# Kernel tuning notes

Hardware: AMD Instinct MI355X
Metric: run time of the kernel (lower is better)

Reference implementation:

```python
import jax, jax.numpy as jnp
import numpy as np

B, D, S, SE, H, DFF = 4, 1024, 1024, 1024, 16, 4096
DH = D // H
NUDGE = 1e-7


def norm(x):
    # x: [B, D, S]; custom layer norm: mean over (1,2), then divide by full L2 norm
    size = x.shape[1] * x.shape[2]
    mean = jnp.sum(x, axis=(1, 2)) / size
    x = x - mean[:, None, None]
    std = jnp.sqrt(jnp.sum(x * x, axis=(1, 2)))
    return x / (std[:, None, None] + NUDGE)


def mha(q_in, kv_in, Wq, Wk, Wv, Wo, causal):
    # q_in: [B, Sq, D], kv_in: [B, Sk, D]
    Bq, Sq, _ = q_in.shape
    Sk = kv_in.shape[1]
    q = (q_in @ Wq).reshape(Bq, Sq, H, DH)
    k = (kv_in @ Wk).reshape(Bq, Sk, H, DH)
    v = (kv_in @ Wv).reshape(Bq, Sk, H, DH)
    scores = jnp.einsum('bqhd,bkhd->bhqk', q, k) / jnp.sqrt(jnp.asarray(DH, q.dtype))
    if causal:
        mask = jnp.tril(jnp.ones((Sq, Sk), dtype=bool))
        scores = jnp.where(mask, scores, jnp.finfo(scores.dtype).min)
    attn = jax.nn.softmax(scores, axis=-1)
    out = jnp.einsum('bhqk,bkhd->bqhd', attn, v).reshape(Bq, Sq, D)
    return out @ Wo


def setup_inputs() -> dict:
    key = jax.random.key(0)
    ks = jax.random.split(key, 13)
    w = lambda k, sh: jax.random.normal(k, sh, dtype=jnp.float32) * 0.02
    return {
        'embedding': jax.random.normal(ks[0], (B, D, SE), dtype=jnp.float32),
        'other_inputs': jax.random.normal(ks[1], (B, D, S), dtype=jnp.float32),
        'Wq_s': w(ks[2], (D, D)), 'Wk_s': w(ks[3], (D, D)),
        'Wv_s': w(ks[4], (D, D)), 'Wo_s': w(ks[5], (D, D)),
        'Wq_c': w(ks[6], (D, D)), 'Wk_c': w(ks[7], (D, D)),
        'Wv_c': w(ks[8], (D, D)), 'Wo_c': w(ks[9], (D, D)),
        'W1': w(ks[10], (D, DFF)), 'b1': jnp.zeros((DFF,), jnp.float32),
        'W2': w(ks[11], (DFF, D)), 'b2': jnp.zeros((D,), jnp.float32),
    }


def reference(embedding, other_inputs, Wq_s, Wk_s, Wv_s, Wo_s,
              Wq_c, Wk_c, Wv_c, Wo_c, W1, b1, W2, b2):
    # tensors are [B, D, S]; attention operates on [B, S, D]
    x = other_inputs.transpose(0, 2, 1)
    sa = mha(x, x, Wq_s, Wk_s, Wv_s, Wo_s, causal=True)
    post_attention = norm(other_inputs + sa.transpose(0, 2, 1))

    pa = post_attention.transpose(0, 2, 1)
    emb = embedding.transpose(0, 2, 1)
    ca = mha(pa, emb, Wq_c, Wk_c, Wv_c, Wo_c, causal=False)
    post_embedding = norm(post_attention + ca.transpose(0, 2, 1))

    # per-token MLP (original loops over axis 2 and restacks; here fully batched)
    pe = post_embedding.transpose(0, 2, 1)  # [B, S, D]
    ff = jax.nn.relu(pe @ W1 + b1) @ W2 + b2
    return norm(post_embedding + ff.transpose(0, 2, 1))
```

## Files before the change

### kernel.cpp

```cpp
#include <hip/hip_runtime.h>
#include <cmath>

#define B_   4
#define D_   1024
#define S_   1024
#define H_   16
#define DH_  64
#define DFF_ 4096

typedef __attribute__((ext_vector_type(8))) short bf16x8;
typedef __attribute__((ext_vector_type(4))) float f32x4;

__device__ __forceinline__ unsigned short f2b(float f) {
    unsigned int u = __float_as_uint(f);
    u += 0x7fffu + ((u >> 16) & 1u);
    return (unsigned short)(u >> 16);
}

__device__ __forceinline__ void gload_lds16(const unsigned short* g, unsigned short* l) {
    __builtin_amdgcn_global_load_lds(
        (const __attribute__((address_space(1))) void*)g,
        (__attribute__((address_space(3))) void*)l, 16, 0, 0);
}

template <int BM, int BN, bool RES>
__global__ __launch_bounds__(256, 2)
void gemm_t(const unsigned short* __restrict__ A,
            const unsigned short* __restrict__ Wt,
            const float* __restrict__ bias,
            const float* __restrict__ residual,
            float* __restrict__ Cf, unsigned short* __restrict__ Cb,
            float* __restrict__ partial,
            int N, int K, int lda, int ldb, long csplit, int relu)
{
    constexpr int FM = BM / 32, FN = BN / 32;
    __shared__ unsigned short As[BM * 64];
    __shared__ unsigned short Bs[BN * 64];
    const int tid = threadIdx.x;
    const int w = tid >> 6, lane = tid & 63;
    const int quad = lane >> 4, l16 = lane & 15;
    const int m0 = blockIdx.x * BM, n0 = blockIdx.y * BN;
    const int wm = (w >> 1) * (BM / 2), wn = (w & 1) * (BN / 2);
    const int srow = lane >> 3;
    const int scol = ((lane & 7) ^ srow) * 8;

    A  += (size_t)blockIdx.z * K;
    Wt += (size_t)blockIdx.z * K;
    if (Cf) Cf += (size_t)blockIdx.z * csplit;

    f32x4 acc[FM][FN] = {};

    for (int k0 = 0; k0 < K; k0 += 64) {
#pragma unroll
        for (int i = 0; i < BM / 32; ++i) {
            const int inst = w + 4 * i;
            gload_lds16(A + (size_t)(m0 + inst * 8 + srow) * lda + k0 + scol,
                        As + inst * 512);
        }
#pragma unroll
        for (int i = 0; i < BN / 32; ++i) {
            const int inst = w + 4 * i;
            gload_lds16(Wt + (size_t)(n0 + inst * 8 + srow) * ldb + k0 + scol,
                        Bs + inst * 512);
        }
        __syncthreads();

#pragma unroll
        for (int kk = 0; kk < 2; ++kk) {
            bf16x8 af[FM], bfr[FN];
#pragma unroll
            for (int i = 0; i < FM; ++i) {
                const int r = wm + i * 16 + l16;
                af[i] = *(const bf16x8*)&As[r * 64 + (((kk * 4 + quad) ^ (r & 7)) * 8)];
            }
#pragma unroll
            for (int j = 0; j < FN; ++j) {
                const int r = wn + j * 16 + l16;
                bfr[j] = *(const bf16x8*)&Bs[r * 64 + (((kk * 4 + quad) ^ (r & 7)) * 8)];
            }
#pragma unroll
            for (int i = 0; i < FM; ++i)
#pragma unroll
                for (int j = 0; j < FN; ++j)
                    acc[i][j] = __builtin_amdgcn_mfma_f32_16x16x32_bf16(af[i], bfr[j], acc[i][j], 0, 0, 0);
        }
        __syncthreads();
    }

    float s = 0.f, ss = 0.f;
#pragma unroll
    for (int i = 0; i < FM; ++i) {
        const int grow = m0 + wm + i * 16 + quad * 4;
#pragma unroll
        for (int j = 0; j < FN; ++j) {
            const int gcol = n0 + wn + j * 16 + l16;
            const float bv = bias ? bias[gcol] : 0.f;
#pragma unroll
            for (int r = 0; r < 4; ++r) {
                float vv = acc[i][j][r] + bv;
                if (relu) vv = fmaxf(vv, 0.f);
                if constexpr (RES) {
                    vv += residual[(size_t)(grow + r) * N + gcol];
                    s += vv; ss += vv * vv;
                    Cf[(size_t)(grow + r) * N + gcol] = vv;
                } else {
                    if (Cf) Cf[(size_t)(grow + r) * N + gcol] = vv;
                    if (Cb) Cb[(size_t)(grow + r) * N + gcol] = f2b(vv);
                }
            }
        }
    }

    if constexpr (RES) {
        float* rs = (float*)As;
        float* rss = rs + 256;
        rs[tid] = s; rss[tid] = ss;
        __syncthreads();
        for (int off = 128; off > 0; off >>= 1) {
            if (tid < off) { rs[tid] += rs[tid + off]; rss[tid] += rss[tid + off]; }
            __syncthreads();
        }
        if (tid == 0) {
            constexpr int YPB = S_ / BM;
            const int b = blockIdx.x / YPB;
            const int chunk = (blockIdx.x % YPB) * gridDim.y + blockIdx.y;
            const int chunks = YPB * gridDim.y;
            partial[((size_t)b * chunks + chunk) * 2 + 0] = rs[0];
            partial[((size_t)b * chunks + chunk) * 2 + 1] = rss[0];
        }
    }
}

__global__ void reduce2_res(const float* __restrict__ pc, const float* __restrict__ res,
                            const float* __restrict__ bias, float* __restrict__ y,
                            float* __restrict__ partial)
{
    const size_t pcs = (size_t)4096 * 1024;
    const int b = blockIdx.y;
    const size_t base = (size_t)b * 1048576 + (size_t)blockIdx.x * 16384;
    float s = 0.f, ss = 0.f;
    for (int i = threadIdx.x; i < 4096; i += 256) {
        const size_t e = base + (size_t)i * 4;
        float4 v0 = *(const float4*)&pc[e];
        float4 v1 = *(const float4*)&pc[e + pcs];
        float4 rv = *(const float4*)&res[e];
        float4 bv = *(const float4*)&bias[e & 1023];
        float4 o;
        o.x = v0.x + v1.x + rv.x + bv.x;
        o.y = v0.y + v1.y + rv.y + bv.y;
        o.z = v0.z + v1.z + rv.z + bv.z;
        o.w = v0.w + v1.w + rv.w + bv.w;
        *(float4*)&y[e] = o;
        s += o.x + o.y + o.z + o.w;
        ss += o.x * o.x + o.y * o.y + o.z * o.z + o.w * o.w;
    }
    __shared__ float rs[256], rss[256];
    rs[threadIdx.x] = s; rss[threadIdx.x] = ss;
    __syncthreads();
    for (int off = 128; off > 0; off >>= 1) {
        if (threadIdx.x < off) {
            rs[threadIdx.x] += rs[threadIdx.x + off];
            rss[threadIdx.x] += rss[threadIdx.x + off];
        }
        __syncthreads();
    }
    if (threadIdx.x == 0) {
        partial[((size_t)b * 64 + blockIdx.x) * 2 + 0] = rs[0];
        partial[((size_t)b * 64 + blockIdx.x) * 2 + 1] = rss[0];
    }
}

__device__ __forceinline__ void stats_reduce(const float* __restrict__ partial,
                                             int b, int chunks, int tid,
                                             float* rs, float* rss,
                                             float& mean, float& inv)
{
    float s = 0.f, ss = 0.f;
    for (int i = tid; i < chunks; i += 256) {
        s  += partial[((size_t)b * chunks + i) * 2 + 0];
        ss += partial[((size_t)b * chunks + i) * 2 + 1];
    }
    rs[tid] = s; rss[tid] = ss;
    __syncthreads();
    for (int off = 128; off > 0; off >>= 1) {
        if (tid < off) { rs[tid] += rs[tid + off]; rss[tid] += rss[tid + off]; }
        __syncthreads();
    }
    const float size = (float)(D_ * S_);
    const float m = rs[0] / size;
    const float var = fmaxf(rss[0] - size * m * m, 0.f);
    mean = m;
    inv = 1.f / (sqrtf(var) + 1e-7f);
    __syncthreads();
}

__global__ void norm_apply_dual(float* __restrict__ y, unsigned short* __restrict__ yb,
                                const float* __restrict__ partial, int chunks)
{
    __shared__ float rs[256], rss[256];
    const int b = blockIdx.y;
    float mean, inv;
    stats_reduce(partial, b, chunks, threadIdx.x, rs, rss, mean, inv);

    const int perBatch = D_ * S_;
    float4* y4 = (float4*)(y + (size_t)b * perBatch);
    unsigned short* yb_ = yb + (size_t)b * perBatch;
    const int n4 = perBatch / 4;
    for (int i = blockIdx.x * blockDim.x + threadIdx.x; i < n4;
         i += gridDim.x * blockDim.x) {
        float4 v = y4[i];
        v.x = (v.x - mean) * inv; v.y = (v.y - mean) * inv;
        v.z = (v.z - mean) * inv; v.w = (v.w - mean) * inv;
        y4[i] = v;
        ushort4 hh; hh.x = f2b(v.x); hh.y = f2b(v.y); hh.z = f2b(v.z); hh.w = f2b(v.w);
        *(ushort4*)(yb_ + (size_t)i * 4) = hh;
    }
}

template <bool CAUSAL>
__global__ __launch_bounds__(256, 2)
void attn_mfma3(const unsigned short* __restrict__ q, const unsigned short* __restrict__ k,
                const unsigned short* __restrict__ vt, unsigned short* __restrict__ o,
                int qstride, int kstride)
{
    __shared__ unsigned short Ks[128 * 64];
    __shared__ unsigned short Vt[64 * 128];
    __shared__ unsigned short Ps[4][2][16][72];
    const int tid = threadIdx.x;
    const int w = tid >> 6, lane = tid & 63;
    const int quad = lane >> 4, l16 = lane & 15;
    const int h = blockIdx.y, b = blockIdx.z;
    const int qt = CAUSAL ? ((blockIdx.x + h) & 7) : blockIdx.x;
    const int q0 = qt * 128;

    const int ksr = lane >> 3, ksc = ((lane & 7) ^ (lane >> 3)) * 8;
    const int vsr = lane >> 4, vsc = lane & 15;

    const unsigned short* qA = q + (size_t)(b * S_ + q0 + w * 16 + l16) * qstride + h * DH_;
    const unsigned short* qB = qA + (size_t)64 * qstride;
    const bf16x8 qa0 = *(const bf16x8*)(qA + quad * 8);
    const bf16x8 qa1 = *(const bf16x8*)(qA + 32 + quad * 8);
    const bf16x8 qb0 = *(const bf16x8*)(qB + quad * 8);
    const bf16x8 qb1 = *(const bf16x8*)(qB + 32 + quad * 8);

    f32x4 OA[4] = {}, OB[4] = {};
    float lA[4] = {}, lB[4] = {};

    const int nit = CAUSAL ? (qt + 1) : (S_ / 128);
    for (int t = 0; t < nit; ++t) {
        const int j0 = t * 128;
#pragma unroll
        for (int i = 0; i < 4; ++i) {
            const int ins = w + 4 * i;
            gload_lds16(k + (size_t)(b * S_ + j0 + ins * 8 + ksr) * kstride + h * DH_ + ksc,
                        Ks + ins * 512);
            const int vrow = ins * 4 + vsr;
            gload_lds16(vt + (size_t)((b * H_ + h) * DH_ + vrow) * S_ + j0
                           + ((vsc ^ (vrow & 15)) * 8),
                        Vt + ins * 512);
        }
        __syncthreads();

#pragma unroll
        for (int g = 0; g < 2; ++g) {
            const int kb = 2 * t + g;
            const int jg = j0 + g * 64;
            const bool doA = !CAUSAL || (kb <= 2 * qt);
            const bool diagA = CAUSAL && (kb == 2 * qt);
            const bool diagB = CAUSAL && (kb == 2 * qt + 1);

            f32x4 stA[4], stB[4];
#pragma unroll
            for (int n = 0; n < 4; ++n) {
                const int kr = g * 64 + n * 16 + l16;
                const bf16x8 kf0 = *(const bf16x8*)&Ks[kr * 64 + ((quad ^ (kr & 7)) * 8)];
                const bf16x8 kf1 = *(const bf16x8*)&Ks[kr * 64 + (((quad + 4) ^ (kr & 7)) * 8)];
                if (doA) {
                    f32x4 c = {};
                    c = __builtin_amdgcn_mfma_f32_16x16x32_bf16(qa0, kf0, c, 0, 0, 0);
                    c = __builtin_amdgcn_mfma_f32_16x16x32_bf16(qa1, kf1, c, 0, 0, 0);
                    stA[n] = c;
                }
                f32x4 c = {};
                c = __builtin_amdgcn_mfma_f32_16x16x32_bf16(qb0, kf0, c, 0, 0, 0);
                c = __builtin_amdgcn_mfma_f32_16x16x32_bf16(qb1, kf1, c, 0, 0, 0);
                stB[n] = c;
            }

            if (doA) {
#pragma unroll
                for (int n = 0; n < 4; ++n)
#pragma unroll
                    for (int r = 0; r < 4; ++r) {
                        float sv = stA[n][r] * 0.125f;
                        if (diagA) {
                            const int row = q0 + w * 16 + quad * 4 + r;
                            const int key = jg + n * 16 + l16;
                            if (key > row) sv = -1e30f;
                        }
                        const float p = __expf(sv);
                        lA[r] += p;
                        Ps[w][0][quad * 4 + r][n * 16 + l16] = f2b(p);
                    }
            }
#pragma unroll
            for (int n = 0; n < 4; ++n)
#pragma unroll
                for (int r = 0; r < 4; ++r) {
                    float sv = stB[n][r] * 0.125f;
                    if (diagB) {
                        const int row = q0 + 64 + w * 16 + quad * 4 + r;
                        const int key = jg + n * 16 + l16;
                        if (key > row) sv = -1e30f;
                    }
                    const float p = __expf(sv);
                    lB[r] += p;
                    Ps[w][1][quad * 4 + r][n * 16 + l16] = f2b(p);
                }
            __threadfence_block();

            const bf16x8 pa0 = *(const bf16x8*)&Ps[w][0][l16][quad * 8];
            const bf16x8 pa1 = *(const bf16x8*)&Ps[w][0][l16][32 + quad * 8];
            const bf16x8 pb0 = *(const bf16x8*)&Ps[w][1][l16][quad * 8];
            const bf16x8 pb1 = *(const bf16x8*)&Ps[w][1][l16][32 + quad * 8];
#pragma unroll
            for (int n = 0; n < 4; ++n) {
                const int vr = n * 16 + l16;
                const bf16x8 vf0 = *(const bf16x8*)&Vt[vr * 128 + (((g * 8 + quad) ^ l16) * 8)];
                const bf16x8 vf1 = *(const bf16x8*)&Vt[vr * 128 + (((g * 8 + quad + 4) ^ l16) * 8)];
                if (doA) {
                    OA[n] = __builtin_amdgcn_mfma_f32_16x16x32_bf16(pa0, vf0, OA[n], 0, 0, 0);
                    OA[n] = __builtin_amdgcn_mfma_f32_16x16x32_bf16(pa1, vf1, OA[n], 0, 0, 0);
                }
                OB[n] = __builtin_amdgcn_mfma_f32_16x16x32_bf16(pb0, vf0, OB[n], 0, 0, 0);
                OB[n] = __builtin_amdgcn_mfma_f32_16x16x32_bf16(pb1, vf1, OB[n], 0, 0, 0);
            }
        }
        __syncthreads();
    }

#pragma unroll
    for (int r = 0; r < 4; ++r) {
        float la = lA[r], lb = lB[r];
        la += __shfl_xor(la, 1); la += __shfl_xor(la, 2);
        la += __shfl_xor(la, 4); la += __shfl_xor(la, 8);
        lb += __shfl_xor(lb, 1); lb += __shfl_xor(lb, 2);
        lb += __shfl_xor(lb, 4); lb += __shfl_xor(lb, 8);
        const float ia = 1.f / la, ib = 1.f / lb;
        const size_t baseA = (size_t)(b * S_ + q0 + w * 16 + quad * 4 + r) * D_ + h * DH_;
        const size_t baseB = baseA + (size_t)64 * D_;
#pragma unroll
        for (int n = 0; n < 4; ++n) {
            o[baseA + n * 16 + l16] = f2b(OA[n][r] * ia);
            o[baseB + n * 16 + l16] = f2b(OB[n][r] * ib);
        }
    }
}

__global__ void transpose_v(const unsigned short* __restrict__ src,
                            unsigned short* __restrict__ dst, int istride)
{
    __shared__ unsigned short t[32][34];
    const int z = blockIdx.z, b = z >> 4, h = z & 15;
    const int s0 = blockIdx.x * 32, d0 = blockIdx.y * 32;
    const int tx = threadIdx.x, ty = threadIdx.y;
#pragma unroll
    for (int i = 0; i < 4; ++i)
        t[ty + i * 8][tx] =
            src[(size_t)(b * S_ + s0 + ty + i * 8) * istride + h * DH_ + d0 + tx];
    __syncthreads();
#pragma unroll
    for (int i = 0; i < 4; ++i)
        dst[(size_t)(z * DH_ + d0 + ty + i * 8) * S_ + s0 + tx] = t[tx][ty + i * 8];
}

struct WJob { const float* src; int sld; long doff; int dld; };
struct WJobs { WJob j[16]; };

__global__ void wtrans_all(WJobs js, unsigned short* __restrict__ dst)
{
    __shared__ float tile[32][33];
    const WJob J = js.j[blockIdx.z];
    const int c0 = blockIdx.x * 32, r0 = blockIdx.y * 32;
    const int tx = threadIdx.x, ty = threadIdx.y;
#pragma unroll
    for (int i = 0; i < 4; ++i)
        tile[ty + i * 8][tx] = J.src[(size_t)(r0 + ty + i * 8) * J.sld + c0 + tx];
    __syncthreads();
#pragma unroll
    for (int i = 0; i < 4; ++i)
        dst[J.doff + (size_t)(c0 + ty + i * 8) * J.dld + r0 + tx] =
            f2b(tile[tx][ty + i * 8]);
}

__global__ void transpose_in(const float* __restrict__ other, const float* __restrict__ emb,
                             float* __restrict__ f0, unsigned short* __restrict__ xb,
                             unsigned short* __restrict__ eb)
{
    __shared__ float tile[32][33];
    const int z = blockIdx.z;
    const int b = z & 3;
    const bool isEmb = z >= 4;
    const float* ip = (isEmb ? emb : other) + (size_t)b * 1048576;
    const int c0 = blockIdx.x * 32, r0 = blockIdx.y * 32;
    const int tx = threadIdx.x, ty = threadIdx.y;
#pragma unroll
    for (int i = 0; i < 4; ++i)
        tile[ty + i * 8][tx] = ip[(size_t)(r0 + ty + i * 8) * 1024 + c0 + tx];
    __syncthreads();
#pragma unroll
    for (int i = 0; i < 4; ++i) {
        const float v = tile[tx][ty + i * 8];
        const size_t oidx = (size_t)b * 1048576 + (size_t)(c0 + ty + i * 8) * 1024 + r0 + tx;
        if (isEmb) eb[oidx] = f2b(v);
        else { f0[oidx] = v; xb[oidx] = f2b(v); }
    }
}

__global__ void transpose_out(const float* __restrict__ in, float* __restrict__ outf,
                              const float* __restrict__ partial, int chunks)
{
    __shared__ float tile[32][33];
    __shared__ float rs[256], rss[256];
    const int z = blockIdx.z;
    const int tx = threadIdx.x, ty = threadIdx.y;
    const int tid = ty * 32 + tx;

    float mean, inv;
    stats_reduce(partial, z, chunks, tid, rs, rss, mean, inv);

    const float* ip = in + (size_t)z * 1048576;
    const int c0 = blockIdx.x * 32, r0 = blockIdx.y * 32;
#pragma unroll
    for (int i = 0; i < 4; ++i)
        tile[ty + i * 8][tx] = ip[(size_t)(r0 + ty + i * 8) * 1024 + c0 + tx];
    __syncthreads();
#pragma unroll
    for (int i = 0; i < 4; ++i) {
        const float v = (tile[tx][ty + i * 8] - mean) * inv;
        outf[(size_t)z * 1048576 + (size_t)(c0 + ty + i * 8) * 1024 + r0 + tx] = v;
    }
}

extern "C" void kernel_launch(void* const* d_in, const int* in_sizes, int n_in,
                              void* d_out, int out_size, void* d_ws, size_t ws_size,
                              hipStream_t stream)
{
    const float* embedding = (const float*)d_in[0];
    const float* other     = (const float*)d_in[1];
    const float* W1 = (const float*)d_in[10];
    const float* b1 = (const float*)d_in[11];
    const float* W2 = (const float*)d_in[12];
    const float* b2 = (const float*)d_in[13];
    float* out = (float*)d_out;

    char* wsb = (char*)d_ws;
    const size_t MB = 1u << 20;
    float* f0 = (float*)(wsb + 0 * MB);
    float* f2 = (float*)(wsb + 16 * MB);
    unsigned short* wts  = (unsigned short*)(wsb + 32 * MB);
    unsigned short* wqkv = wts;
    unsigned short* wo_s = wts + 3 * 1048576;
    unsigned short* wq_c = wts + 4 * 1048576;
    unsigned short* wkv_c= wts + 5 * 1048576;
    unsigned short* wo_c = wts + 7 * 1048576;
    unsigned short* w1t  = wts + 8 * 1048576;
    unsigned short* w2t  = wts + 12 * 1048576;
    unsigned short* actA = (unsigned short*)(wsb + 64 * MB);
    unsigned short* actB = (unsigned short*)(wsb + 72 * MB);
    unsigned short* actC = (unsigned short*)(wsb + 80 * MB);
    unsigned short* actC2 = actC + 4 * 1048576;
    unsigned short* aout  = actC + 12 * 1048576;
    float* pc      = (float*)(wsb + 112 * MB);
    float* partial = (float*)(wsb + 176 * MB);

    const dim3 blkT(32, 8), blk256(256);
    const dim3 gAttn(S_ / 128, H_, B_);
    const dim3 gVt(32, 2, B_ * H_);
    const dim3 gApply(64, B_);

    WJobs js;
    for (int z = 0; z < 8; ++z)
        js.j[z] = { (const float*)d_in[2 + z], 1024, (long)z * 1048576, 1024 };
    for (int q = 0; q < 4; ++q)
        js.j[8 + q] = { W1 + (size_t)q * 1024, 4096, (long)(8 + q) * 1048576, 1024 };
    for (int q = 0; q < 4; ++q)
        js.j[12 + q] = { W2 + (size_t)q * 1048576, 1024, 12L * 1048576 + q * 1024, 4096 };
    hipLaunchKernelGGL(wtrans_all, dim3(32, 32, 16), blkT, 0, stream, js, wts);

    hipLaunchKernelGGL(transpose_in, dim3(32, 32, 8), blkT, 0, stream,
                       other, embedding, f0, actA, actB);

    hipLaunchKernelGGL((gemm_t<128, 128, false>), dim3(32, 24), blk256, 0, stream,
                       actA, wqkv, nullptr, nullptr, nullptr, actC, nullptr,
                       3072, 1024, 1024, 1024, 0L, 0);
    hipLaunchKernelGGL(transpose_v, gVt, blkT, 0, stream, actC + 2048, actA, 3072);
    hipLaunchKernelGGL(attn_mfma3<true>, gAttn, blk256, 0, stream,
                       actC, actC + 1024, actA, aout, 3072, 3072);
    hipLaunchKernelGGL((gemm_t<64, 128, true>), dim3(64, 8), blk256, 0, stream,
                       aout, wo_s, nullptr, f0, f2, nullptr, partial,
                       1024, 1024, 1024, 1024, 0L, 0);
    hipLaunchKernelGGL(norm_apply_dual, gApply, blk256, 0, stream, f2, actA, partial, 128);

    hipLaunchKernelGGL((gemm_t<64, 128, false>), dim3(64, 8), blk256, 0, stream,
                       actA, wq_c, nullptr, nullptr, nullptr, actC, nullptr,
                       1024, 1024, 1024, 1024, 0L, 0);
    hipLaunchKernelGGL((gemm_t<128, 128, false>), dim3(32, 16), blk256, 0, stream,
                       actB, wkv_c, nullptr, nullptr, nullptr, actC2, nullptr,
                       2048, 1024, 1024, 1024, 0L, 0);
    hipLaunchKernelGGL(transpose_v, gVt, blkT, 0, stream, actC2 + 1024, actB, 2048);
    hipLaunchKernelGGL(attn_mfma3<false>, gAttn, blk256, 0, stream,
                       actC, actC2, actB, aout, 1024, 2048);
    hipLaunchKernelGGL((gemm_t<64, 128, true>), dim3(64, 8), blk256, 0, stream,
                       aout, wo_c, nullptr, f2, f0, nullptr, partial,
                       1024, 1024, 1024, 1024, 0L, 0);
    hipLaunchKernelGGL(norm_apply_dual, gApply, blk256, 0, stream, f0, actA, partial, 128);

    hipLaunchKernelGGL((gemm_t<128, 128, false>), dim3(32, 32), blk256, 0, stream,
                       actA, w1t, b1, nullptr, nullptr, actC, nullptr,
                       DFF_, 1024, 1024, 1024, 0L, 1);
    hipLaunchKernelGGL((gemm_t<128, 128, false>), dim3(32, 8, 2), blk256, 0, stream,
                       actC, w2t, nullptr, nullptr, pc, nullptr, nullptr,
                       1024, 2048, 4096, 4096, (long)4096 * 1024, 0);
    hipLaunchKernelGGL(reduce2_res, gApply, blk256, 0, stream, pc, f0, b2, f2, partial);
    hipLaunchKernelGGL(transpose_out, dim3(32, 32, B_), blkT, 0, stream, f2, out, partial, 64);

    (void)in_sizes; (void)n_in; (void)out_size; (void)ws_size;
}
```

Before: 503.5 us.

## Split attention query tile across 8 waves instead of 4 with two sub-tiles each

```diff
diff --git a/kernel.cpp b/kernel.cpp
--- a/kernel.cpp
+++ b/kernel.cpp
@@ -218,40 +218,38 @@
 }
 
 template <bool CAUSAL>
-__global__ __launch_bounds__(256, 2)
+__global__ __launch_bounds__(512, 4)
 void attn_mfma3(const unsigned short* __restrict__ q, const unsigned short* __restrict__ k,
                 const unsigned short* __restrict__ vt, unsigned short* __restrict__ o,
                 int qstride, int kstride)
 {
     __shared__ unsigned short Ks[128 * 64];
     __shared__ unsigned short Vt[64 * 128];
-    __shared__ unsigned short Ps[4][2][16][72];
+    __shared__ unsigned short Ps[8][16][72];
     const int tid = threadIdx.x;
     const int w = tid >> 6, lane = tid & 63;
     const int quad = lane >> 4, l16 = lane & 15;
     const int h = blockIdx.y, b = blockIdx.z;
     const int qt = CAUSAL ? ((blockIdx.x + h) & 7) : blockIdx.x;
     const int q0 = qt * 128;
+    const int row0 = q0 + w * 16;
 
     const int ksr = lane >> 3, ksc = ((lane & 7) ^ (lane >> 3)) * 8;
     const int vsr = lane >> 4, vsc = lane & 15;
 
-    const unsigned short* qA = q + (size_t)(b * S_ + q0 + w * 16 + l16) * qstride + h * DH_;
-    const unsigned short* qB = qA + (size_t)64 * qstride;
+    const unsigned short* qA = q + (size_t)(b * S_ + row0 + l16) * qstride + h * DH_;
     const bf16x8 qa0 = *(const bf16x8*)(qA + quad * 8);
     const bf16x8 qa1 = *(const bf16x8*)(qA + 32 + quad * 8);
-    const bf16x8 qb0 = *(const bf16x8*)(qB + quad * 8);
-    const bf16x8 qb1 = *(const bf16x8*)(qB + 32 + quad * 8);
-
-    f32x4 OA[4] = {}, OB[4] = {};
-    float lA[4] = {}, lB[4] = {};
+
+    f32x4 OA[4] = {};
+    float lA[4] = {};
 
     const int nit = CAUSAL ? (qt + 1) : (S_ / 128);
     for (int t = 0; t < nit; ++t) {
         const int j0 = t * 128;
 #pragma unroll
-        for (int i = 0; i < 4; ++i) {
-            const int ins = w + 4 * i;
+        for (int i = 0; i < 2; ++i) {
+            const int ins = w + 8 * i;
             gload_lds16(k + (size_t)(b * S_ + j0 + ins * 8 + ksr) * kstride + h * DH_ + ksc,
                         Ks + ins * 512);
             const int vrow = ins * 4 + vsr;
@@ -263,77 +261,49 @@
 
 #pragma unroll
         for (int g = 0; g < 2; ++g) {
-            const int kb = 2 * t + g;
             const int jg = j0 + g * 64;
-            const bool doA = !CAUSAL || (kb <= 2 * qt);
-            const bool diagA = CAUSAL && (kb == 2 * qt);
-            const bool diagB = CAUSAL && (kb == 2 * qt + 1);
-
-            f32x4 stA[4], stB[4];
-#pragma unroll
-            for (int n = 0; n < 4; ++n) {
-                const int kr = g * 64 + n * 16 + l16;
-                const bf16x8 kf0 = *(const bf16x8*)&Ks[kr * 64 + ((quad ^ (kr & 7)) * 8)];
-                const bf16x8 kf1 = *(const bf16x8*)&Ks[kr * 64 + (((quad + 4) ^ (kr & 7)) * 8)];
-                if (doA) {
+            const bool doW = !CAUSAL || (jg <= row0 + 15);
+            const bool needMask = CAUSAL && doW && (jg + 63 > row0);
+
+            if (doW) {
+                f32x4 stA[4];
+#pragma unroll
+                for (int n = 0; n < 4; ++n) {
+                    const int kr = g * 64 + n * 16 + l16;
+                    const bf16x8 kf0 = *(const bf16x8*)&Ks[kr * 64 + ((quad ^ (kr & 7)) * 8)];
+                    const bf16x8 kf1 = *(const bf16x8*)&Ks[kr * 64 + (((quad + 4) ^ (kr & 7)) * 8)];
                     f32x4 c = {};
                     c = __builtin_amdgcn_mfma_f32_16x16x32_bf16(qa0, kf0, c, 0, 0, 0);
                     c = __builtin_amdgcn_mfma_f32_16x16x32_bf16(qa1, kf1, c, 0, 0, 0);
                     stA[n] = c;
                 }
-                f32x4 c = {};
-                c = __builtin_amdgcn_mfma_f32_16x16x32_bf16(qb0, kf0, c, 0, 0, 0);
-                c = __builtin_amdgcn_mfma_f32_16x16x32_bf16(qb1, kf1, c, 0, 0, 0);
-                stB[n] = c;
-            }
-
-            if (doA) {
+
 #pragma unroll
                 for (int n = 0; n < 4; ++n)
 #pragma unroll
                     for (int r = 0; r < 4; ++r) {
                         float sv = stA[n][r] * 0.125f;
-                        if (diagA) {
-                            const int row = q0 + w * 16 + quad * 4 + r;
+                        if (needMask) {
+                            const int row = row0 + quad * 4 + r;
                             const int key = jg + n * 16 + l16;
                             if (key > row) sv = -1e30f;
                         }
                         const float p = __expf(sv);
                         lA[r] += p;
-                        Ps[w][0][quad * 4 + r][n * 16 + l16] = f2b(p);
+                        Ps[w][quad * 4 + r][n * 16 + l16] = f2b(p);
                     }
-            }
-#pragma unroll
-            for (int n = 0; n < 4; ++n)
-#pragma unroll
-                for (int r = 0; r < 4; ++r) {
-                    float sv = stB[n][r] * 0.125f;
-                    if (diagB) {
-                        const int row = q0 + 64 + w * 16 + quad * 4 + r;
-                        const int key = jg + n * 16 + l16;
-                        if (key > row) sv = -1e30f;
-                    }
-                    const float p = __expf(sv);
-                    lB[r] += p;
-                    Ps[w][1][quad * 4 + r][n * 16 + l16] = f2b(p);
-                }
-            __threadfence_block();
-
-            const bf16x8 pa0 = *(const bf16x8*)&Ps[w][0][l16][quad * 8];
-            const bf16x8 pa1 = *(const bf16x8*)&Ps[w][0][l16][32 + quad * 8];
-            const bf16x8 pb0 = *(const bf16x8*)&Ps[w][1][l16][quad * 8];
-            const bf16x8 pb1 = *(const bf16x8*)&Ps[w][1][l16][32 + quad * 8];
-#pragma unroll
-            for (int n = 0; n < 4; ++n) {
-                const int vr = n * 16 + l16;
-                const bf16x8 vf0 = *(const bf16x8*)&Vt[vr * 128 + (((g * 8 + quad) ^ l16) * 8)];
-                const bf16x8 vf1 = *(const bf16x8*)&Vt[vr * 128 + (((g * 8 + quad + 4) ^ l16) * 8)];
-                if (doA) {
+                __threadfence_block();
+
+                const bf16x8 pa0 = *(const bf16x8*)&Ps[w][l16][quad * 8];
+                const bf16x8 pa1 = *(const bf16x8*)&Ps[w][l16][32 + quad * 8];
+#pragma unroll
+                for (int n = 0; n < 4; ++n) {
+                    const int vr = n * 16 + l16;
+                    const bf16x8 vf0 = *(const bf16x8*)&Vt[vr * 128 + (((g * 8 + quad) ^ l16) * 8)];
+                    const bf16x8 vf1 = *(const bf16x8*)&Vt[vr * 128 + (((g * 8 + quad + 4) ^ l16) * 8)];
                     OA[n] = __builtin_amdgcn_mfma_f32_16x16x32_bf16(pa0, vf0, OA[n], 0, 0, 0);
                     OA[n] = __builtin_amdgcn_mfma_f32_16x16x32_bf16(pa1, vf1, OA[n], 0, 0, 0);
                 }
-                OB[n] = __builtin_amdgcn_mfma_f32_16x16x32_bf16(pb0, vf0, OB[n], 0, 0, 0);
-                OB[n] = __builtin_amdgcn_mfma_f32_16x16x32_bf16(pb1, vf1, OB[n], 0, 0, 0);
             }
         }
         __syncthreads();
@@ -341,19 +311,14 @@
 
 #pragma unroll
     for (int r = 0; r < 4; ++r) {
-        float la = lA[r], lb = lB[r];
+        float la = lA[r];
         la += __shfl_xor(la, 1); la += __shfl_xor(la, 2);
         la += __shfl_xor(la, 4); la += __shfl_xor(la, 8);
-        lb += __shfl_xor(lb, 1); lb += __shfl_xor(lb, 2);
-        lb += __shfl_xor(lb, 4); lb += __shfl_xor(lb, 8);
-        const float ia = 1.f / la, ib = 1.f / lb;
-        const size_t baseA = (size_t)(b * S_ + q0 + w * 16 + quad * 4 + r) * D_ + h * DH_;
-        const size_t baseB = baseA + (size_t)64 * D_;
-#pragma unroll
-        for (int n = 0; n < 4; ++n) {
+        const float ia = 1.f / la;
+        const size_t baseA = (size_t)(b * S_ + row0 + quad * 4 + r) * D_ + h * DH_;
+#pragma unroll
+        for (int n = 0; n < 4; ++n)
             o[baseA + n * 16 + l16] = f2b(OA[n][r] * ia);
-            o[baseB + n * 16 + l16] = f2b(OB[n][r] * ib);
-        }
     }
 }
 
@@ -474,7 +439,7 @@
     float* pc      = (float*)(wsb + 112 * MB);
     float* partial = (float*)(wsb + 176 * MB);
 
-    const dim3 blkT(32, 8), blk256(256);
+    const dim3 blkT(32, 8), blk256(256), blk512(512);
     const dim3 gAttn(S_ / 128, H_, B_);
     const dim3 gVt(32, 2, B_ * H_);
     const dim3 gApply(64, B_);
@@ -495,7 +460,7 @@
                        actA, wqkv, nullptr, nullptr, nullptr, actC, nullptr,
                        3072, 1024, 1024, 1024, 0L, 0);
     hipLaunchKernelGGL(transpose_v, gVt, blkT, 0, stream, actC + 2048, actA, 3072);
-    hipLaunchKernelGGL(attn_mfma3<true>, gAttn, blk256, 0, stream,
+    hipLaunchKernelGGL(attn_mfma3<true>, gAttn, blk512, 0, stream,
                        actC, actC + 1024, actA, aout, 3072, 3072);
     hipLaunchKernelGGL((gemm_t<64, 128, true>), dim3(64, 8), blk256, 0, stream,
                        aout, wo_s, nullptr, f0, f2, nullptr, partial,
@@ -509,7 +474,7 @@
                        actB, wkv_c, nullptr, nullptr, nullptr, actC2, nullptr,
                        2048, 1024, 1024, 1024, 0L, 0);
     hipLaunchKernelGGL(transpose_v, gVt, blkT, 0, stream, actC2 + 1024, actB, 2048);
-    hipLaunchKernelGGL(attn_mfma3<false>, gAttn, blk256, 0, stream,
+    hipLaunchKernelGGL(attn_mfma3<false>, gAttn, blk512, 0, stream,
                        actC, actC2, actB, aout, 1024, 2048);
     hipLaunchKernelGGL((gemm_t<64, 128, true>), dim3(64, 8), blk256, 0, stream,
                        aout, wo_c, nullptr, f2, f0, nullptr, partial,
```

Result: faster. 467.7 us (-7.1%).
